# Optimization experiments

Hardware: AMD Instinct MI355X
Metric: run time of the kernel (lower is better)

Reference implementation:

```python
import jax, jax.numpy as jnp
import numpy as np

N = 50_000
E = 1_600_000
C_IN, C_HID, C_OUT, M = 128, 128, 2, 4


def gcn_norm(edge_index, num_nodes):
    # GCNConv default: add self-loops, symmetric normalization D^-1/2 (A+I) D^-1/2
    src, dst = edge_index[0], edge_index[1]
    loop = jnp.arange(num_nodes, dtype=edge_index.dtype)
    src = jnp.concatenate([src, loop])
    dst = jnp.concatenate([dst, loop])
    deg = jax.ops.segment_sum(jnp.ones_like(dst, dtype=jnp.float32), dst,
                              num_segments=num_nodes)
    dinv = jnp.where(deg > 0, jax.lax.rsqrt(deg), 0.0)
    norm = dinv[src] * dinv[dst]  # [E+N]
    return src, dst, norm


def propagate(h, src, dst, norm, num_nodes):
    # gather -> scale -> scatter-add (the memory-bound core)
    return jax.ops.segment_sum(h[src] * norm[:, None], dst, num_segments=num_nodes)


def setup_inputs() -> dict:
    key = jax.random.key(0)
    k0, k1, k2, k3 = jax.random.split(key, 4)
    x = jax.random.normal(k0, (N, C_IN), dtype=jnp.float32)
    edge_index = jax.random.randint(k1, (2, E), 0, N, dtype=jnp.int32)
    W1 = jax.random.normal(k2, (C_IN, C_HID), dtype=jnp.float32) * (1.0 / np.sqrt(C_IN))
    b1 = jnp.zeros((C_HID,), dtype=jnp.float32)
    W_out = jax.random.normal(k3, (M, C_HID, C_OUT), dtype=jnp.float32) * (1.0 / np.sqrt(C_HID))
    b_out = jnp.zeros((M, C_OUT), dtype=jnp.float32)
    return {"x": x, "edge_index": edge_index, "W1": W1, "b1": b1,
            "W_out": W_out, "b_out": b_out}


def reference(x, edge_index, W1, b1, W_out, b_out):
    n = x.shape[0]
    src, dst, norm = gcn_norm(edge_index, n)
    # hidden GCNConv + ReLU
    h = x @ W1                                  # [N, C_HID]
    h = propagate(h, src, dst, norm, n) + b1    # [N, C_HID]
    h = jax.nn.relu(h)
    # m output GCNConv heads. GCN propagation is linear in features, so
    # A_hat(h W_m) == (A_hat h) W_m: share one graph traversal across heads.
    agg = propagate(h, src, dst, norm, n)       # [N, C_HID]
    out = jnp.einsum('nf,mfo->mno', agg, W_out) + b_out[:, None, :]  # [M, N, C_OUT]
    return out
```

## Files before the change

### kernel.cpp

```cpp
#include <hip/hip_runtime.h>


constexpr int CIN = 128;
constexpr int BSHIFT = 6;
constexpr int NBLKB = 256;
constexpr int NBUK_MAX = 1024;
constexpr int CSR_CAP = 4096;

typedef __attribute__((ext_vector_type(8))) short short8v;
typedef __attribute__((ext_vector_type(4))) float float4v;

__device__ inline unsigned pack_bf16x2(float a, float b) {
  unsigned ua = __float_as_uint(a), ub = __float_as_uint(b);
  ua = (ua + 0x7FFFu + ((ua >> 16) & 1u)) >> 16;
  ub = (ub + 0x7FFFu + ((ub >> 16) & 1u)) >> 16;
  return ua | (ub << 16);
}
__device__ inline float bf_lo(unsigned u) { return __uint_as_float(u << 16); }
__device__ inline float bf_hi(unsigned u) { return __uint_as_float(u & 0xFFFF0000u); }

__global__ __launch_bounds__(256) void histbuck_k(const int* __restrict__ dst,
    int* __restrict__ blockhist, int E, int nbuk) {
  __shared__ int lh[NBUK_MAX];
  int b = blockIdx.x, t = threadIdx.x;
  for (int k = t; k < nbuk; k += 256) lh[k] = 0;
  __syncthreads();
  int per = (E + gridDim.x - 1) / gridDim.x;
  int s0 = b * per, s1 = min(E, s0 + per);
  for (int i = s0 + t; i < s1; i += 256) atomicAdd(&lh[dst[i] >> BSHIFT], 1);
  __syncthreads();
  for (int k = t; k < nbuk; k += 256) blockhist[k * NBLKB + b] = lh[k];
}

__global__ void scan_k(const int* __restrict__ v_in,
    int* __restrict__ excl_out, int* __restrict__ btot, int n) {
  __shared__ int wsum[16];
  int t = threadIdx.x, l = t & 63, w = t >> 6;
  int nw = blockDim.x >> 6;
  int i = blockIdx.x * blockDim.x + t;
  int v = (i < n) ? v_in[i] : 0;
  int orig = v;
  #pragma unroll
  for (int off = 1; off < 64; off <<= 1) {
    int u = __shfl_up(v, off);
    if (l >= off) v += u;
  }
  if (l == 63) wsum[w] = v;
  __syncthreads();
  int add = 0;
  for (int j = 0; j < nw; ++j) if (j < w) add += wsum[j];
  v += add;
  if (i < n) excl_out[i] = v - orig;
  if (t == (int)blockDim.x - 1 && btot != nullptr) btot[blockIdx.x] = v;
}

__global__ __launch_bounds__(256) void stageB_k(const int* __restrict__ src,
    const int* __restrict__ dst, const int* __restrict__ soff,
    const int* __restrict__ boff, unsigned* __restrict__ stage, int E, int nbuk) {
  __shared__ int loff[NBUK_MAX];
  int b = blockIdx.x, t = threadIdx.x;
  for (int k = t; k < nbuk; k += 256) loff[k] = soff[k * NBLKB + b] + boff[k];
  __syncthreads();
  int per = (E + gridDim.x - 1) / gridDim.x;
  int s0 = b * per, s1 = min(E, s0 + per);
  for (int i = s0 + t; i < s1; i += 256) {
    int d = dst[i], s = src[i];
    int pos = atomicAdd(&loff[d >> BSHIFT], 1);
    stage[pos] = (unsigned)s | ((unsigned)(d & 63) << 17);
  }
}

__global__ __launch_bounds__(256) void csrloc_k(const unsigned* __restrict__ stage,
    const int* __restrict__ soff, const int* __restrict__ boff,
    int* __restrict__ row_ptr, int* __restrict__ csr,
    float* __restrict__ dinv, int N, int E, int nbuk) {
  __shared__ int cnt64[64], off64[64], cur64[64];
  __shared__ unsigned ebuf[CSR_CAP];
  __shared__ int sbuf[CSR_CAP];
  int k = blockIdx.x, t = threadIdx.x;
  if (t < 64) { cnt64[t] = 0; cur64[t] = 0; }
  __syncthreads();
  int r0 = soff[k * NBLKB] + boff[k];
  int r1 = (k + 1 < nbuk) ? soff[(k + 1) * NBLKB] + boff[k + 1] : E;
  int len = r1 - r0;
  if (len <= CSR_CAP) {
    for (int i = t; i < len; i += 256) {
      unsigned s = stage[r0 + i];
      ebuf[i] = s;
      atomicAdd(&cnt64[s >> 17], 1);
    }
    __syncthreads();
    if (t < 64) {
      int v = cnt64[t], orig = v;
      #pragma unroll
      for (int off = 1; off < 64; off <<= 1) {
        int u = __shfl_up(v, off);
        if (t >= off) v += u;
      }
      off64[t] = v - orig;
      int n = (k << BSHIFT) + t;
      if (n < N) {
        row_ptr[n] = r0 + v - orig;
        dinv[n] = rsqrtf((float)(orig + 1));
      }
      if (k == nbuk - 1 && t == 63) row_ptr[N] = E;
    }
    __syncthreads();
    for (int i = t; i < len; i += 256) {
      unsigned s = ebuf[i];
      int dl = s >> 17;
      int pos = off64[dl] + atomicAdd(&cur64[dl], 1);
      sbuf[pos] = (int)(s & 0x1FFFF);
    }
    __syncthreads();
    for (int i = t; i < len; i += 256) csr[r0 + i] = sbuf[i];
  } else {
    for (int i = r0 + t; i < r1; i += 256) atomicAdd(&cnt64[stage[i] >> 17], 1);
    __syncthreads();
    if (t < 64) {
      int v = cnt64[t], orig = v;
      #pragma unroll
      for (int off = 1; off < 64; off <<= 1) {
        int u = __shfl_up(v, off);
        if (t >= off) v += u;
      }
      off64[t] = v - orig;
      int n = (k << BSHIFT) + t;
      if (n < N) {
        row_ptr[n] = r0 + v - orig;
        dinv[n] = rsqrtf((float)(orig + 1));
      }
      if (k == nbuk - 1 && t == 63) row_ptr[N] = E;
    }
    __syncthreads();
    for (int i = r0 + t; i < r1; i += 256) {
      unsigned s = stage[i];
      int dl = s >> 17;
      int pos = r0 + off64[dl] + atomicAdd(&cur64[dl], 1);
      csr[pos] = (int)(s & 0x1FFFF);
    }
  }
}

__device__ inline void split8(const float* f, short8v& ah, short8v& al) {
  #pragma unroll
  for (int j = 0; j < 8; ++j) {
    unsigned ua = __float_as_uint(f[j]);
    unsigned hb = (ua + 0x7FFFu + ((ua >> 16) & 1u)) >> 16;
    float fh = __uint_as_float(hb << 16);
    float rl = f[j] - fh;
    unsigned ub = __float_as_uint(rl);
    unsigned lb = (ub + 0x7FFFu + ((ub >> 16) & 1u)) >> 16;
    ah[j] = (short)hb;
    al[j] = (short)lb;
  }
}

__global__ __launch_bounds__(256) void gemm_k(const float* __restrict__ x,
    const float* __restrict__ W, const float* __restrict__ dinv,
    unsigned* __restrict__ gu, int nrows) {
  __shared__ unsigned short Bh[16384];
  __shared__ unsigned short Bl[16384];
  int t = threadIdx.x, l = t & 63, w = t >> 6;
  for (int idx = t; idx < 16384; idx += 256) {
    int k = idx >> 7, col = idx & 127;
    float wv = W[idx];
    unsigned ua = __float_as_uint(wv);
    unsigned hb = (ua + 0x7FFFu + ((ua >> 16) & 1u)) >> 16;
    float fh = __uint_as_float(hb << 16);
    float rl = wv - fh;
    unsigned ub = __float_as_uint(rl);
    unsigned lb = (ub + 0x7FFFu + ((ub >> 16) & 1u)) >> 16;
    int addr = (((k >> 5) * 8 + (col >> 4)) * 64 +
                (((k >> 3) & 3) * 16 + (col & 15))) * 8 + (k & 7);
    Bh[addr] = (unsigned short)hb;
    Bl[addr] = (unsigned short)lb;
  }
  __syncthreads();

  int row0 = blockIdx.x * 128;
  int ct0 = w * 2;
  float4v acc[8][2];
  #pragma unroll
  for (int i = 0; i < 8; ++i) { acc[i][0] = (float4v)0.f; acc[i][1] = (float4v)0.f; }
  int arow = row0 + (l & 15);
  int kln = (l >> 4) * 8;

  for (int ks = 0; ks < 4; ++ks) {
    short8v bh0 = *(short8v*)&Bh[((ks * 8 + ct0) * 64 + l) * 8];
    short8v bh1 = *(short8v*)&Bh[((ks * 8 + ct0 + 1) * 64 + l) * 8];
    short8v bl0 = *(short8v*)&Bl[((ks * 8 + ct0) * 64 + l) * 8];
    short8v bl1 = *(short8v*)&Bl[((ks * 8 + ct0 + 1) * 64 + l) * 8];
    #pragma unroll
    for (int rt = 0; rt < 8; ++rt) {
      int r = arow + rt * 16;
      const float* xp = &x[(size_t)min(r, nrows - 1) * CIN + ks * 32 + kln];
      float f[8];
      *(float4*)&f[0] = *(const float4*)xp;
      *(float4*)&f[4] = *(const float4*)(xp + 4);
      short8v ah, al;
      split8(f, ah, al);
      acc[rt][0] = __builtin_amdgcn_mfma_f32_16x16x32_bf16(ah, bh0, acc[rt][0], 0, 0, 0);
      acc[rt][1] = __builtin_amdgcn_mfma_f32_16x16x32_bf16(ah, bh1, acc[rt][1], 0, 0, 0);
      acc[rt][0] = __builtin_amdgcn_mfma_f32_16x16x32_bf16(ah, bl0, acc[rt][0], 0, 0, 0);
      acc[rt][1] = __builtin_amdgcn_mfma_f32_16x16x32_bf16(ah, bl1, acc[rt][1], 0, 0, 0);
      acc[rt][0] = __builtin_amdgcn_mfma_f32_16x16x32_bf16(al, bh0, acc[rt][0], 0, 0, 0);
      acc[rt][1] = __builtin_amdgcn_mfma_f32_16x16x32_bf16(al, bh1, acc[rt][1], 0, 0, 0);
    }
  }
  #pragma unroll
  for (int rt = 0; rt < 8; ++rt) {
    #pragma unroll
    for (int r = 0; r < 4; ++r) {
      int row = row0 + rt * 16 + (l >> 4) * 4 + r;
      bool ok = row < nrows;
      float dv = ok ? dinv[row] : 0.f;
      #pragma unroll
      for (int c = 0; c < 2; ++c) {
        float val = acc[rt][c][r] * dv;
        float other = __shfl_xor(val, 1);
        int col = (ct0 + c) * 16 + (l & 15);
        if (ok && !(l & 1)) gu[(size_t)row * 64 + (col >> 1)] = pack_bf16x2(val, other);
      }
    }
  }
}

#define ACC8(U) do { \
  acc[0] += bf_lo((U).x); acc[1] += bf_hi((U).x); \
  acc[2] += bf_lo((U).y); acc[3] += bf_hi((U).y); \
  acc[4] += bf_lo((U).z); acc[5] += bf_hi((U).z); \
  acc[6] += bf_lo((U).w); acc[7] += bf_hi((U).w); } while (0)

__global__ __launch_bounds__(256) void prop1_k(const uint4* __restrict__ g4,
    const int* __restrict__ row_ptr, const int* __restrict__ csr,
    const float* __restrict__ dinv, const float* __restrict__ b1,
    const float* __restrict__ Wout, unsigned* __restrict__ g2w,
    int n_nodes, int n_waves) {
  int l = threadIdx.x & 63;
  int q = l & 15, sub = l >> 4;
  int wid = (blockIdx.x * blockDim.x + threadIdx.x) >> 6;
  float wj0[8], wj1[8], bb[8];
  #pragma unroll
  for (int c = 0; c < 8; ++c) {
    int col = 8 * q + c;
    wj0[c] = Wout[sub * 256 + col * 2];
    wj1[c] = Wout[sub * 256 + col * 2 + 1];
    bb[c] = b1[col];
  }
  for (int n = wid; n < n_nodes; n += n_waves) {
    int start = row_ptr[n], end = row_ptr[n + 1];
    float d = dinv[n];
    float acc[8];
    #pragma unroll
    for (int c = 0; c < 8; ++c) acc[c] = 0.f;
    for (int base = start; base < end; base += 64) {
      int cnt = min(64, end - base);
      int eb = (base + l < end) ? csr[base + l] : 0;
      int i = 0;
      for (; i + 16 <= cnt; i += 16) {
        int s0 = __shfl(eb, i + sub);
        int s1 = __shfl(eb, i + 4 + sub);
        int s2 = __shfl(eb, i + 8 + sub);
        int s3 = __shfl(eb, i + 12 + sub);
        uint4 u0 = g4[s0 * 16 + q];
        uint4 u1 = g4[s1 * 16 + q];
        uint4 u2 = g4[s2 * 16 + q];
        uint4 u3 = g4[s3 * 16 + q];
        ACC8(u0); ACC8(u1); ACC8(u2); ACC8(u3);
      }
      for (; i + 4 <= cnt; i += 4) {
        int s0 = __shfl(eb, i + sub);
        uint4 u0 = g4[s0 * 16 + q];
        ACC8(u0);
      }
      if (i < cnt) {
        int idx = i + sub;
        bool vld = idx < cnt;
        int s0 = __shfl(eb, vld ? idx : i);
        uint4 u0 = g4[s0 * 16 + q];
        if (vld) { ACC8(u0); }
      }
    }
    #pragma unroll
    for (int c = 0; c < 8; ++c) {
      acc[c] += __shfl_xor(acc[c], 16);
      acc[c] += __shfl_xor(acc[c], 32);
    }
    uint4 us = g4[n * 16 + q];
    ACC8(us);
    float p0 = 0.f, p1 = 0.f;
    #pragma unroll
    for (int c = 0; c < 8; ++c) {
      float y = fmaxf(fmaf(acc[c], d, bb[c]), 0.f);
      p0 = fmaf(y, wj0[c], p0);
      p1 = fmaf(y, wj1[c], p1);
    }
    #pragma unroll
    for (int off = 1; off < 16; off <<= 1) {
      p0 += __shfl_xor(p0, off);
      p1 += __shfl_xor(p1, off);
    }
    if (q == 0) g2w[n * 4 + sub] = pack_bf16x2(d * p0, d * p1);
  }
}

__global__ __launch_bounds__(256) void prop2_k(const uint2* __restrict__ g2v,
    const int* __restrict__ row_ptr, const int* __restrict__ csr,
    const float* __restrict__ dinv, const float* __restrict__ bout,
    float* __restrict__ out, int N) {
  int tid = blockIdx.x * 256 + threadIdx.x;
  int n = tid >> 1, hf = tid & 1;
  if (n >= N) return;
  uint2 us = g2v[n * 2 + hf];
  float a0 = bf_lo(us.x), a1 = bf_hi(us.x);
  float a2 = bf_lo(us.y), a3 = bf_hi(us.y);
  int e = row_ptr[n], e1 = row_ptr[n + 1];
  for (; e + 4 <= e1; e += 4) {
    int i0 = csr[e], i1 = csr[e + 1], i2 = csr[e + 2], i3 = csr[e + 3];
    uint2 u0 = g2v[i0 * 2 + hf], u1 = g2v[i1 * 2 + hf];
    uint2 u2 = g2v[i2 * 2 + hf], u3 = g2v[i3 * 2 + hf];
    a0 += (bf_lo(u0.x) + bf_lo(u1.x)) + (bf_lo(u2.x) + bf_lo(u3.x));
    a1 += (bf_hi(u0.x) + bf_hi(u1.x)) + (bf_hi(u2.x) + bf_hi(u3.x));
    a2 += (bf_lo(u0.y) + bf_lo(u1.y)) + (bf_lo(u2.y) + bf_lo(u3.y));
    a3 += (bf_hi(u0.y) + bf_hi(u1.y)) + (bf_hi(u2.y) + bf_hi(u3.y));
  }
  for (; e < e1; ++e) {
    uint2 u = g2v[csr[e] * 2 + hf];
    a0 += bf_lo(u.x); a1 += bf_hi(u.x);
    a2 += bf_lo(u.y); a3 += bf_hi(u.y);
  }
  float d = dinv[n];
  float2 o0 = make_float2(fmaf(d, a0, bout[hf * 4 + 0]), fmaf(d, a1, bout[hf * 4 + 1]));
  float2 o1 = make_float2(fmaf(d, a2, bout[hf * 4 + 2]), fmaf(d, a3, bout[hf * 4 + 3]));
  *(float2*)&out[(size_t)(hf * 2 + 0) * (2 * N) + 2 * n] = o0;
  *(float2*)&out[(size_t)(hf * 2 + 1) * (2 * N) + 2 * n] = o1;
}

extern "C" void kernel_launch(void* const* d_in, const int* in_sizes, int n_in,
                              void* d_out, int out_size, void* d_ws, size_t ws_size,
                              hipStream_t stream) {
  const float* x    = (const float*)d_in[0];
  const int*   ei   = (const int*)d_in[1];
  const float* W1   = (const float*)d_in[2];
  const float* b1   = (const float*)d_in[3];
  const float* Wout = (const float*)d_in[4];
  const float* bout = (const float*)d_in[5];
  float* out = (float*)d_out;

  const int N = in_sizes[0] / CIN;
  const int E = in_sizes[1] / 2;
  const int* srcp = ei;
  const int* dstp = ei + E;
  const int NBUK = (N + 63) >> BSHIFT;
  const int NSC = NBUK * NBLKB;

  char* ws = (char*)d_ws;
  size_t off = 0;
  auto alloc = [&](size_t bytes) -> void* {
    void* p = ws + off;
    off = (off + bytes + 511) & ~(size_t)511;
    return p;
  };
  unsigned*       gu        = (unsigned*)alloc((size_t)N * 64 * 4);
  unsigned short* g2u       = (unsigned short*)alloc((size_t)N * 8 * 2);
  float*          dinv      = (float*)alloc((size_t)N * 4);
  int*            blockhist = (int*)alloc((size_t)NSC * 4);
  int*            soff      = (int*)alloc((size_t)NSC * 4);
  int*            btot      = (int*)alloc((size_t)NBUK_MAX * 4);
  int*            boff      = (int*)alloc((size_t)NBUK_MAX * 4);
  int*            row_ptr   = (int*)alloc((size_t)(N + 1) * 4);
  int*            csr       = (int*)alloc((size_t)E * 4);
  unsigned*       stage     = (unsigned*)alloc((size_t)E * 4);
  (void)ws_size; (void)n_in; (void)out_size;

  histbuck_k<<<NBLKB, 256, 0, stream>>>(dstp, blockhist, E, NBUK);
  scan_k<<<NBUK, 256, 0, stream>>>(blockhist, soff, btot, NSC);
  scan_k<<<1, 1024, 0, stream>>>(btot, boff, nullptr, NBUK);
  stageB_k<<<NBLKB, 256, 0, stream>>>(srcp, dstp, soff, boff, stage, E, NBUK);
  csrloc_k<<<NBUK, 256, 0, stream>>>(stage, soff, boff, row_ptr, csr, dinv, N, E, NBUK);

  gemm_k<<<(N + 127) / 128, 256, 0, stream>>>(x, W1, dinv, gu, N);

  const int P1_BLOCKS = 2048;
  prop1_k<<<P1_BLOCKS, 256, 0, stream>>>((const uint4*)gu, row_ptr, csr, dinv, b1,
                                         Wout, (unsigned*)g2u, N, P1_BLOCKS * 4);
  prop2_k<<<(2 * N + 255) / 256, 256, 0, stream>>>((const uint2*)g2u, row_ptr, csr,
                                                   dinv, bout, out, N);
}
```

Baseline: 144.1 us.

## Slice hidden features into column panels for cache-local gather and coarsen CSR buckets

The GEMM output is stored as 8 column slices of 16 bf16 features per node, so each gather in the first propagation touches a smaller per-slice table that fits better in L2/LLC. Each block processes one slice, and a new finalize kernel reduces the per-slice partial head projections. CSR construction also moves from 64-node to 256-node buckets with a larger LDS staging buffer. In exchange, the edge list is traversed 8 times, gathers become 32-bit per lane instead of 128-bit, and an fp32 partial buffer plus an extra kernel launch are added.

```diff
diff --git a/kernel.cpp b/kernel.cpp
--- a/kernel.cpp
+++ b/kernel.cpp
@@ -2,10 +2,9 @@
 
 
 constexpr int CIN = 128;
-constexpr int BSHIFT = 6;
+constexpr int SSHIFT = 8;
 constexpr int NBLKB = 256;
-constexpr int NBUK_MAX = 1024;
-constexpr int CSR_CAP = 4096;
+constexpr int CSR_CAP = 10240;
 
 typedef __attribute__((ext_vector_type(8))) short short8v;
 typedef __attribute__((ext_vector_type(4))) float float4v;
@@ -19,17 +18,17 @@
 __device__ inline float bf_lo(unsigned u) { return __uint_as_float(u << 16); }
 __device__ inline float bf_hi(unsigned u) { return __uint_as_float(u & 0xFFFF0000u); }
 
-__global__ __launch_bounds__(256) void histbuck_k(const int* __restrict__ dst,
-    int* __restrict__ blockhist, int E, int nbuk) {
-  __shared__ int lh[NBUK_MAX];
+__global__ __launch_bounds__(256) void histsb_k(const int* __restrict__ dst,
+    int* __restrict__ blockhist, int E, int nsb) {
+  __shared__ int lh[256];
   int b = blockIdx.x, t = threadIdx.x;
-  for (int k = t; k < nbuk; k += 256) lh[k] = 0;
+  lh[t] = 0;
   __syncthreads();
   int per = (E + gridDim.x - 1) / gridDim.x;
   int s0 = b * per, s1 = min(E, s0 + per);
-  for (int i = s0 + t; i < s1; i += 256) atomicAdd(&lh[dst[i] >> BSHIFT], 1);
-  __syncthreads();
-  for (int k = t; k < nbuk; k += 256) blockhist[k * NBLKB + b] = lh[k];
+  for (int i = s0 + t; i < s1; i += 256) atomicAdd(&lh[dst[i] >> SSHIFT], 1);
+  __syncthreads();
+  if (t < nsb) blockhist[t * NBLKB + b] = lh[t];
 }
 
 __global__ void scan_k(const int* __restrict__ v_in,
@@ -56,87 +55,80 @@
 
 __global__ __launch_bounds__(256) void stageB_k(const int* __restrict__ src,
     const int* __restrict__ dst, const int* __restrict__ soff,
-    const int* __restrict__ boff, unsigned* __restrict__ stage, int E, int nbuk) {
-  __shared__ int loff[NBUK_MAX];
+    const int* __restrict__ boff, unsigned* __restrict__ stage, int E, int nsb) {
+  __shared__ int loff[256];
   int b = blockIdx.x, t = threadIdx.x;
-  for (int k = t; k < nbuk; k += 256) loff[k] = soff[k * NBLKB + b] + boff[k];
+  if (t < nsb) loff[t] = soff[t * NBLKB + b] + boff[t];
   __syncthreads();
   int per = (E + gridDim.x - 1) / gridDim.x;
   int s0 = b * per, s1 = min(E, s0 + per);
   for (int i = s0 + t; i < s1; i += 256) {
     int d = dst[i], s = src[i];
-    int pos = atomicAdd(&loff[d >> BSHIFT], 1);
-    stage[pos] = (unsigned)s | ((unsigned)(d & 63) << 17);
-  }
-}
-
-__global__ __launch_bounds__(256) void csrloc_k(const unsigned* __restrict__ stage,
-    const int* __restrict__ soff, const int* __restrict__ boff,
-    int* __restrict__ row_ptr, int* __restrict__ csr,
-    float* __restrict__ dinv, int N, int E, int nbuk) {
-  __shared__ int cnt64[64], off64[64], cur64[64];
+    int pos = atomicAdd(&loff[d >> SSHIFT], 1);
+    stage[pos] = (unsigned)s | ((unsigned)(d & 255) << 17);
+  }
+}
+
+__global__ __launch_bounds__(256) void csrsb_k(const unsigned* __restrict__ stage,
+    const int* __restrict__ boff, int* __restrict__ row_ptr, int* __restrict__ csr,
+    float* __restrict__ dinv, int N, int E, int nsb) {
+  __shared__ int cnt[256], off[256], cur[256];
   __shared__ unsigned ebuf[CSR_CAP];
   __shared__ int sbuf[CSR_CAP];
-  int k = blockIdx.x, t = threadIdx.x;
-  if (t < 64) { cnt64[t] = 0; cur64[t] = 0; }
-  __syncthreads();
-  int r0 = soff[k * NBLKB] + boff[k];
-  int r1 = (k + 1 < nbuk) ? soff[(k + 1) * NBLKB] + boff[k + 1] : E;
+  __shared__ int wsum[4];
+  int k = blockIdx.x, t = threadIdx.x, l = t & 63, w = t >> 6;
+  cnt[t] = 0; cur[t] = 0;
+  __syncthreads();
+  int r0 = boff[k];
+  int r1 = (k + 1 < nsb) ? boff[k + 1] : E;
   int len = r1 - r0;
-  if (len <= CSR_CAP) {
+  bool fits = len <= CSR_CAP;
+  if (fits) {
     for (int i = t; i < len; i += 256) {
       unsigned s = stage[r0 + i];
       ebuf[i] = s;
-      atomicAdd(&cnt64[s >> 17], 1);
-    }
+      atomicAdd(&cnt[s >> 17], 1);
+    }
+  } else {
+    for (int i = r0 + t; i < r1; i += 256) atomicAdd(&cnt[stage[i] >> 17], 1);
+  }
+  __syncthreads();
+  {
+    int v = cnt[t], orig = v;
+    #pragma unroll
+    for (int o = 1; o < 64; o <<= 1) {
+      int u = __shfl_up(v, o);
+      if (l >= o) v += u;
+    }
+    if (l == 63) wsum[w] = v;
     __syncthreads();
-    if (t < 64) {
-      int v = cnt64[t], orig = v;
-      #pragma unroll
-      for (int off = 1; off < 64; off <<= 1) {
-        int u = __shfl_up(v, off);
-        if (t >= off) v += u;
-      }
-      off64[t] = v - orig;
-      int n = (k << BSHIFT) + t;
-      if (n < N) {
-        row_ptr[n] = r0 + v - orig;
-        dinv[n] = rsqrtf((float)(orig + 1));
-      }
-      if (k == nbuk - 1 && t == 63) row_ptr[N] = E;
-    }
-    __syncthreads();
+    int add = 0;
+    #pragma unroll
+    for (int j = 0; j < 4; ++j) if (j < w) add += wsum[j];
+    int excl = v + add - orig;
+    off[t] = excl;
+    int n = (k << SSHIFT) + t;
+    if (n < N) {
+      row_ptr[n] = r0 + excl;
+      dinv[n] = rsqrtf((float)(orig + 1));
+    }
+    if (k == nsb - 1 && t == 255) row_ptr[N] = E;
+  }
+  __syncthreads();
+  if (fits) {
     for (int i = t; i < len; i += 256) {
       unsigned s = ebuf[i];
       int dl = s >> 17;
-      int pos = off64[dl] + atomicAdd(&cur64[dl], 1);
+      int pos = off[dl] + atomicAdd(&cur[dl], 1);
       sbuf[pos] = (int)(s & 0x1FFFF);
     }
     __syncthreads();
     for (int i = t; i < len; i += 256) csr[r0 + i] = sbuf[i];
   } else {
-    for (int i = r0 + t; i < r1; i += 256) atomicAdd(&cnt64[stage[i] >> 17], 1);
-    __syncthreads();
-    if (t < 64) {
-      int v = cnt64[t], orig = v;
-      #pragma unroll
-      for (int off = 1; off < 64; off <<= 1) {
-        int u = __shfl_up(v, off);
-        if (t >= off) v += u;
-      }
-      off64[t] = v - orig;
-      int n = (k << BSHIFT) + t;
-      if (n < N) {
-        row_ptr[n] = r0 + v - orig;
-        dinv[n] = rsqrtf((float)(orig + 1));
-      }
-      if (k == nbuk - 1 && t == 63) row_ptr[N] = E;
-    }
-    __syncthreads();
     for (int i = r0 + t; i < r1; i += 256) {
       unsigned s = stage[i];
       int dl = s >> 17;
-      int pos = r0 + off64[dl] + atomicAdd(&cur64[dl], 1);
+      int pos = r0 + off[dl] + atomicAdd(&cur[dl], 1);
       csr[pos] = (int)(s & 0x1FFFF);
     }
   }
@@ -219,90 +211,86 @@
       for (int c = 0; c < 2; ++c) {
         float val = acc[rt][c][r] * dv;
         float other = __shfl_xor(val, 1);
-        int col = (ct0 + c) * 16 + (l & 15);
-        if (ok && !(l & 1)) gu[(size_t)row * 64 + (col >> 1)] = pack_bf16x2(val, other);
+        int slice = ct0 + c;
+        if (ok && !(l & 1))
+          gu[((size_t)slice * nrows + row) * 8 + ((l & 15) >> 1)] = pack_bf16x2(val, other);
       }
     }
   }
 }
 
-#define ACC8(U) do { \
-  acc[0] += bf_lo((U).x); acc[1] += bf_hi((U).x); \
-  acc[2] += bf_lo((U).y); acc[3] += bf_hi((U).y); \
-  acc[4] += bf_lo((U).z); acc[5] += bf_hi((U).z); \
-  acc[6] += bf_lo((U).w); acc[7] += bf_hi((U).w); } while (0)
-
-__global__ __launch_bounds__(256) void prop1_k(const uint4* __restrict__ g4,
+__global__ __launch_bounds__(256) void prop1s_k(const unsigned* __restrict__ gs,
     const int* __restrict__ row_ptr, const int* __restrict__ csr,
     const float* __restrict__ dinv, const float* __restrict__ b1,
-    const float* __restrict__ Wout, unsigned* __restrict__ g2w,
-    int n_nodes, int n_waves) {
-  int l = threadIdx.x & 63;
-  int q = l & 15, sub = l >> 4;
-  int wid = (blockIdx.x * blockDim.x + threadIdx.x) >> 6;
-  float wj0[8], wj1[8], bb[8];
-  #pragma unroll
-  for (int c = 0; c < 8; ++c) {
-    int col = 8 * q + c;
-    wj0[c] = Wout[sub * 256 + col * 2];
-    wj1[c] = Wout[sub * 256 + col * 2 + 1];
-    bb[c] = b1[col];
-  }
-  for (int n = wid; n < n_nodes; n += n_waves) {
+    const float* __restrict__ Wout, float* __restrict__ g2part,
+    int N, int waves_per_slice) {
+  int slice = blockIdx.x & 7;
+  int chunk = blockIdx.x >> 3;
+  int t = threadIdx.x, l = t & 63, w = t >> 6;
+  int gi = l >> 3, il = l & 7;
+  int c0 = slice * 16 + 2 * il, c1 = c0 + 1;
+  float wa = Wout[(gi >> 1) * 256 + c0 * 2 + (gi & 1)];
+  float wb = Wout[(gi >> 1) * 256 + c1 * 2 + (gi & 1)];
+  float ba = b1[c0], bb2 = b1[c1];
+  const unsigned* gb = gs + (size_t)slice * N * 8 + il;
+  float* gp = g2part + (size_t)slice * N * 8;
+
+  int wsl = chunk * 4 + w;
+  for (int n = wsl; n < N; n += waves_per_slice) {
     int start = row_ptr[n], end = row_ptr[n + 1];
     float d = dinv[n];
-    float acc[8];
-    #pragma unroll
-    for (int c = 0; c < 8; ++c) acc[c] = 0.f;
+    float ax = 0.f, ay = 0.f;
     for (int base = start; base < end; base += 64) {
       int cnt = min(64, end - base);
       int eb = (base + l < end) ? csr[base + l] : 0;
       int i = 0;
       for (; i + 16 <= cnt; i += 16) {
-        int s0 = __shfl(eb, i + sub);
-        int s1 = __shfl(eb, i + 4 + sub);
-        int s2 = __shfl(eb, i + 8 + sub);
-        int s3 = __shfl(eb, i + 12 + sub);
-        uint4 u0 = g4[s0 * 16 + q];
-        uint4 u1 = g4[s1 * 16 + q];
-        uint4 u2 = g4[s2 * 16 + q];
-        uint4 u3 = g4[s3 * 16 + q];
-        ACC8(u0); ACC8(u1); ACC8(u2); ACC8(u3);
+        int sa = __shfl(eb, i + gi);
+        int sb = __shfl(eb, i + 8 + gi);
+        unsigned ua = gb[(size_t)sa * 8];
+        unsigned ub = gb[(size_t)sb * 8];
+        ax += bf_lo(ua) + bf_lo(ub);
+        ay += bf_hi(ua) + bf_hi(ub);
       }
-      for (; i + 4 <= cnt; i += 4) {
-        int s0 = __shfl(eb, i + sub);
-        uint4 u0 = g4[s0 * 16 + q];
-        ACC8(u0);
+      for (; i + 8 <= cnt; i += 8) {
+        int sa = __shfl(eb, i + gi);
+        unsigned ua = gb[(size_t)sa * 8];
+        ax += bf_lo(ua); ay += bf_hi(ua);
       }
       if (i < cnt) {
-        int idx = i + sub;
-        bool vld = idx < cnt;
-        int s0 = __shfl(eb, vld ? idx : i);
-        uint4 u0 = g4[s0 * 16 + q];
-        if (vld) { ACC8(u0); }
+        int idx = i + gi;
+        int sa = __shfl(eb, idx < cnt ? idx : i);
+        if (idx < cnt) {
+          unsigned ua = gb[(size_t)sa * 8];
+          ax += bf_lo(ua); ay += bf_hi(ua);
+        }
       }
     }
-    #pragma unroll
-    for (int c = 0; c < 8; ++c) {
-      acc[c] += __shfl_xor(acc[c], 16);
-      acc[c] += __shfl_xor(acc[c], 32);
-    }
-    uint4 us = g4[n * 16 + q];
-    ACC8(us);
-    float p0 = 0.f, p1 = 0.f;
-    #pragma unroll
-    for (int c = 0; c < 8; ++c) {
-      float y = fmaxf(fmaf(acc[c], d, bb[c]), 0.f);
-      p0 = fmaf(y, wj0[c], p0);
-      p1 = fmaf(y, wj1[c], p1);
-    }
-    #pragma unroll
-    for (int off = 1; off < 16; off <<= 1) {
-      p0 += __shfl_xor(p0, off);
-      p1 += __shfl_xor(p1, off);
-    }
-    if (q == 0) g2w[n * 4 + sub] = pack_bf16x2(d * p0, d * p1);
-  }
+    ax += __shfl_xor(ax, 8); ax += __shfl_xor(ax, 16); ax += __shfl_xor(ax, 32);
+    ay += __shfl_xor(ay, 8); ay += __shfl_xor(ay, 16); ay += __shfl_xor(ay, 32);
+    unsigned us = gb[(size_t)n * 8];
+    ax += bf_lo(us); ay += bf_hi(us);
+    float y0 = fmaxf(fmaf(ax, d, ba), 0.f);
+    float y1 = fmaxf(fmaf(ay, d, bb2), 0.f);
+    float c = fmaf(y0, wa, y1 * wb);
+    c += __shfl_xor(c, 1); c += __shfl_xor(c, 2); c += __shfl_xor(c, 4);
+    if (il == 0) gp[(size_t)n * 8 + gi] = c;
+  }
+}
+
+__global__ __launch_bounds__(256) void finalize_k(const float* __restrict__ g2part,
+    const float* __restrict__ dinv, unsigned* __restrict__ g2w, int N) {
+  int tid = blockIdx.x * 256 + threadIdx.x;
+  if (tid >= N * 4) return;
+  int n = tid >> 2, jp = tid & 3;
+  float s0 = 0.f, s1 = 0.f;
+  #pragma unroll
+  for (int s = 0; s < 8; ++s) {
+    const float* p = &g2part[((size_t)s * N + n) * 8 + jp * 2];
+    s0 += p[0]; s1 += p[1];
+  }
+  float d = dinv[n];
+  g2w[n * 4 + jp] = pack_bf16x2(d * s0, d * s1);
 }
 
 __global__ __launch_bounds__(256) void prop2_k(const uint2* __restrict__ g2v,
@@ -352,8 +340,8 @@
   const int E = in_sizes[1] / 2;
   const int* srcp = ei;
   const int* dstp = ei + E;
-  const int NBUK = (N + 63) >> BSHIFT;
-  const int NSC = NBUK * NBLKB;
+  const int NSB = (N + 255) >> SSHIFT;
+  const int NSC = NSB * NBLKB;
 
   char* ws = (char*)d_ws;
   size_t off = 0;
@@ -363,28 +351,30 @@
     return p;
   };
   unsigned*       gu        = (unsigned*)alloc((size_t)N * 64 * 4);
+  float*          g2part    = (float*)alloc((size_t)8 * N * 8 * 4);
   unsigned short* g2u       = (unsigned short*)alloc((size_t)N * 8 * 2);
   float*          dinv      = (float*)alloc((size_t)N * 4);
   int*            blockhist = (int*)alloc((size_t)NSC * 4);
   int*            soff      = (int*)alloc((size_t)NSC * 4);
-  int*            btot      = (int*)alloc((size_t)NBUK_MAX * 4);
-  int*            boff      = (int*)alloc((size_t)NBUK_MAX * 4);
+  int*            btot      = (int*)alloc(256 * 4);
+  int*            boff      = (int*)alloc(256 * 4);
   int*            row_ptr   = (int*)alloc((size_t)(N + 1) * 4);
   int*            csr       = (int*)alloc((size_t)E * 4);
   unsigned*       stage     = (unsigned*)alloc((size_t)E * 4);
   (void)ws_size; (void)n_in; (void)out_size;
 
-  histbuck_k<<<NBLKB, 256, 0, stream>>>(dstp, blockhist, E, NBUK);
-  scan_k<<<NBUK, 256, 0, stream>>>(blockhist, soff, btot, NSC);
-  scan_k<<<1, 1024, 0, stream>>>(btot, boff, nullptr, NBUK);
-  stageB_k<<<NBLKB, 256, 0, stream>>>(srcp, dstp, soff, boff, stage, E, NBUK);
-  csrloc_k<<<NBUK, 256, 0, stream>>>(stage, soff, boff, row_ptr, csr, dinv, N, E, NBUK);
+  histsb_k<<<NBLKB, 256, 0, stream>>>(dstp, blockhist, E, NSB);
+  scan_k<<<NSB, 256, 0, stream>>>(blockhist, soff, btot, NSC);
+  scan_k<<<1, 256, 0, stream>>>(btot, boff, nullptr, NSB);
+  stageB_k<<<NBLKB, 256, 0, stream>>>(srcp, dstp, soff, boff, stage, E, NSB);
+  csrsb_k<<<NSB, 256, 0, stream>>>(stage, boff, row_ptr, csr, dinv, N, E, NSB);
 
   gemm_k<<<(N + 127) / 128, 256, 0, stream>>>(x, W1, dinv, gu, N);
 
   const int P1_BLOCKS = 2048;
-  prop1_k<<<P1_BLOCKS, 256, 0, stream>>>((const uint4*)gu, row_ptr, csr, dinv, b1,
-                                         Wout, (unsigned*)g2u, N, P1_BLOCKS * 4);
+  prop1s_k<<<P1_BLOCKS, 256, 0, stream>>>(gu, row_ptr, csr, dinv, b1, Wout,
+                                          g2part, N, (P1_BLOCKS / 8) * 4);
+  finalize_k<<<(N * 4 + 255) / 256, 256, 0, stream>>>(g2part, dinv, (unsigned*)g2u, N);
   prop2_k<<<(2 * N + 255) / 256, 256, 0, stream>>>((const uint2*)g2u, row_ptr, csr,
                                                    dinv, bout, out, N);
 }
```

New measurement: 196.1 us. +36.1%, slower.

## Use 256-node superbuckets for CSR build and stage A tiles in LDS

Applied to the files above, without the earlier changes.

The CSR construction now buckets edges by 256-node superbuckets instead of 64-node buckets. This cuts the bucket count to about 196, so the second scan kernel goes away: the bucket-total scan is recomputed inside stageB and the CSR kernel, and the CSR kernel sorts with a 10K-entry LDS buffer. Separately, the GEMM now converts x to bf16 hi/lo once per row into shared memory rather than having each wave reload and split the same x values. The trade-offs are fewer CSR blocks and a larger LDS footprint, which may lower occupancy, plus extra barriers in the GEMM.

```diff
diff --git a/kernel.cpp b/kernel.cpp
--- a/kernel.cpp
+++ b/kernel.cpp
@@ -2,10 +2,9 @@
 
 
 constexpr int CIN = 128;
-constexpr int BSHIFT = 6;
+constexpr int SSHIFT = 8;
 constexpr int NBLKB = 256;
-constexpr int NBUK_MAX = 1024;
-constexpr int CSR_CAP = 4096;
+constexpr int CSR_CAP = 10240;
 
 typedef __attribute__((ext_vector_type(8))) short short8v;
 typedef __attribute__((ext_vector_type(4))) float float4v;
@@ -18,26 +17,34 @@
 }
 __device__ inline float bf_lo(unsigned u) { return __uint_as_float(u << 16); }
 __device__ inline float bf_hi(unsigned u) { return __uint_as_float(u & 0xFFFF0000u); }
-
-__global__ __launch_bounds__(256) void histbuck_k(const int* __restrict__ dst,
-    int* __restrict__ blockhist, int E, int nbuk) {
-  __shared__ int lh[NBUK_MAX];
+__device__ inline void split1(float v, unsigned short& h, unsigned short& lo) {
+  unsigned ua = __float_as_uint(v);
+  unsigned hb = (ua + 0x7FFFu + ((ua >> 16) & 1u)) >> 16;
+  float fh = __uint_as_float(hb << 16);
+  float rl = v - fh;
+  unsigned ub = __float_as_uint(rl);
+  h = (unsigned short)hb;
+  lo = (unsigned short)((ub + 0x7FFFu + ((ub >> 16) & 1u)) >> 16);
+}
+
+__global__ __launch_bounds__(256) void histsb_k(const int* __restrict__ dst,
+    int* __restrict__ blockhist, int E, int nsb) {
+  __shared__ int lh[256];
   int b = blockIdx.x, t = threadIdx.x;
-  for (int k = t; k < nbuk; k += 256) lh[k] = 0;
+  lh[t] = 0;
   __syncthreads();
   int per = (E + gridDim.x - 1) / gridDim.x;
   int s0 = b * per, s1 = min(E, s0 + per);
-  for (int i = s0 + t; i < s1; i += 256) atomicAdd(&lh[dst[i] >> BSHIFT], 1);
-  __syncthreads();
-  for (int k = t; k < nbuk; k += 256) blockhist[k * NBLKB + b] = lh[k];
-}
-
-__global__ void scan_k(const int* __restrict__ v_in,
+  for (int i = s0 + t; i < s1; i += 256) atomicAdd(&lh[dst[i] >> SSHIFT], 1);
+  __syncthreads();
+  if (t < nsb) blockhist[t * NBLKB + b] = lh[t];
+}
+
+__global__ __launch_bounds__(256) void scan_k(const int* __restrict__ v_in,
     int* __restrict__ excl_out, int* __restrict__ btot, int n) {
-  __shared__ int wsum[16];
+  __shared__ int wsum[4];
   int t = threadIdx.x, l = t & 63, w = t >> 6;
-  int nw = blockDim.x >> 6;
-  int i = blockIdx.x * blockDim.x + t;
+  int i = blockIdx.x * 256 + t;
   int v = (i < n) ? v_in[i] : 0;
   int orig = v;
   #pragma unroll
@@ -48,111 +55,114 @@
   if (l == 63) wsum[w] = v;
   __syncthreads();
   int add = 0;
-  for (int j = 0; j < nw; ++j) if (j < w) add += wsum[j];
+  #pragma unroll
+  for (int j = 0; j < 4; ++j) if (j < w) add += wsum[j];
   v += add;
   if (i < n) excl_out[i] = v - orig;
-  if (t == (int)blockDim.x - 1 && btot != nullptr) btot[blockIdx.x] = v;
+  if (t == 255) btot[blockIdx.x] = v;
 }
 
 __global__ __launch_bounds__(256) void stageB_k(const int* __restrict__ src,
     const int* __restrict__ dst, const int* __restrict__ soff,
-    const int* __restrict__ boff, unsigned* __restrict__ stage, int E, int nbuk) {
-  __shared__ int loff[NBUK_MAX];
-  int b = blockIdx.x, t = threadIdx.x;
-  for (int k = t; k < nbuk; k += 256) loff[k] = soff[k * NBLKB + b] + boff[k];
+    const int* __restrict__ btot, unsigned* __restrict__ stage, int E, int nsb) {
+  __shared__ int loff[256];
+  __shared__ int wsum[4];
+  int b = blockIdx.x, t = threadIdx.x, l = t & 63, w = t >> 6;
+  int bv = (t < nsb) ? btot[t] : 0;
+  int vv = bv;
+  #pragma unroll
+  for (int o = 1; o < 64; o <<= 1) { int u = __shfl_up(vv, o); if (l >= o) vv += u; }
+  if (l == 63) wsum[w] = vv;
+  __syncthreads();
+  int add = 0;
+  #pragma unroll
+  for (int j = 0; j < 4; ++j) if (j < w) add += wsum[j];
+  int bexcl = vv + add - bv;
+  if (t < nsb) loff[t] = soff[t * NBLKB + b] + bexcl;
   __syncthreads();
   int per = (E + gridDim.x - 1) / gridDim.x;
   int s0 = b * per, s1 = min(E, s0 + per);
   for (int i = s0 + t; i < s1; i += 256) {
     int d = dst[i], s = src[i];
-    int pos = atomicAdd(&loff[d >> BSHIFT], 1);
-    stage[pos] = (unsigned)s | ((unsigned)(d & 63) << 17);
-  }
-}
-
-__global__ __launch_bounds__(256) void csrloc_k(const unsigned* __restrict__ stage,
-    const int* __restrict__ soff, const int* __restrict__ boff,
-    int* __restrict__ row_ptr, int* __restrict__ csr,
-    float* __restrict__ dinv, int N, int E, int nbuk) {
-  __shared__ int cnt64[64], off64[64], cur64[64];
+    int pos = atomicAdd(&loff[d >> SSHIFT], 1);
+    stage[pos] = (unsigned)s | ((unsigned)(d & 255) << 17);
+  }
+}
+
+__global__ __launch_bounds__(256) void csrsb_k(const unsigned* __restrict__ stage,
+    const int* __restrict__ btot, int* __restrict__ row_ptr, int* __restrict__ csr,
+    float* __restrict__ dinv, int N, int E, int nsb) {
+  __shared__ int cnt[256], off[256], cur[256], sboff[256];
   __shared__ unsigned ebuf[CSR_CAP];
   __shared__ int sbuf[CSR_CAP];
-  int k = blockIdx.x, t = threadIdx.x;
-  if (t < 64) { cnt64[t] = 0; cur64[t] = 0; }
-  __syncthreads();
-  int r0 = soff[k * NBLKB] + boff[k];
-  int r1 = (k + 1 < nbuk) ? soff[(k + 1) * NBLKB] + boff[k + 1] : E;
+  __shared__ int wsum[4];
+  int k = blockIdx.x, t = threadIdx.x, l = t & 63, w = t >> 6;
+  cnt[t] = 0; cur[t] = 0;
+  {
+    int bv = (t < nsb) ? btot[t] : 0;
+    int vv = bv;
+    #pragma unroll
+    for (int o = 1; o < 64; o <<= 1) { int u = __shfl_up(vv, o); if (l >= o) vv += u; }
+    if (l == 63) wsum[w] = vv;
+    __syncthreads();
+    int add = 0;
+    #pragma unroll
+    for (int j = 0; j < 4; ++j) if (j < w) add += wsum[j];
+    sboff[t] = vv + add - bv;
+  }
+  __syncthreads();
+  int r0 = sboff[k];
+  int r1 = (k + 1 < nsb) ? sboff[k + 1] : E;
   int len = r1 - r0;
-  if (len <= CSR_CAP) {
+  bool fits = len <= CSR_CAP;
+  if (fits) {
     for (int i = t; i < len; i += 256) {
       unsigned s = stage[r0 + i];
       ebuf[i] = s;
-      atomicAdd(&cnt64[s >> 17], 1);
-    }
+      atomicAdd(&cnt[s >> 17], 1);
+    }
+  } else {
+    for (int i = r0 + t; i < r1; i += 256) atomicAdd(&cnt[stage[i] >> 17], 1);
+  }
+  __syncthreads();
+  {
+    int v = cnt[t], orig = v;
+    #pragma unroll
+    for (int o = 1; o < 64; o <<= 1) {
+      int u = __shfl_up(v, o);
+      if (l >= o) v += u;
+    }
+    if (l == 63) wsum[w] = v;
     __syncthreads();
-    if (t < 64) {
-      int v = cnt64[t], orig = v;
-      #pragma unroll
-      for (int off = 1; off < 64; off <<= 1) {
-        int u = __shfl_up(v, off);
-        if (t >= off) v += u;
-      }
-      off64[t] = v - orig;
-      int n = (k << BSHIFT) + t;
-      if (n < N) {
-        row_ptr[n] = r0 + v - orig;
-        dinv[n] = rsqrtf((float)(orig + 1));
-      }
-      if (k == nbuk - 1 && t == 63) row_ptr[N] = E;
-    }
-    __syncthreads();
+    int add = 0;
+    #pragma unroll
+    for (int j = 0; j < 4; ++j) if (j < w) add += wsum[j];
+    int excl = v + add - orig;
+    off[t] = excl;
+    int n = (k << SSHIFT) + t;
+    if (n < N) {
+      row_ptr[n] = r0 + excl;
+      dinv[n] = rsqrtf((float)(orig + 1));
+    }
+    if (k == nsb - 1 && t == 255) row_ptr[N] = E;
+  }
+  __syncthreads();
+  if (fits) {
     for (int i = t; i < len; i += 256) {
       unsigned s = ebuf[i];
       int dl = s >> 17;
-      int pos = off64[dl] + atomicAdd(&cur64[dl], 1);
+      int pos = off[dl] + atomicAdd(&cur[dl], 1);
       sbuf[pos] = (int)(s & 0x1FFFF);
     }
     __syncthreads();
     for (int i = t; i < len; i += 256) csr[r0 + i] = sbuf[i];
   } else {
-    for (int i = r0 + t; i < r1; i += 256) atomicAdd(&cnt64[stage[i] >> 17], 1);
-    __syncthreads();
-    if (t < 64) {
-      int v = cnt64[t], orig = v;
-      #pragma unroll
-      for (int off = 1; off < 64; off <<= 1) {
-        int u = __shfl_up(v, off);
-        if (t >= off) v += u;
-      }
-      off64[t] = v - orig;
-      int n = (k << BSHIFT) + t;
-      if (n < N) {
-        row_ptr[n] = r0 + v - orig;
-        dinv[n] = rsqrtf((float)(orig + 1));
-      }
-      if (k == nbuk - 1 && t == 63) row_ptr[N] = E;
-    }
-    __syncthreads();
     for (int i = r0 + t; i < r1; i += 256) {
       unsigned s = stage[i];
       int dl = s >> 17;
-      int pos = r0 + off64[dl] + atomicAdd(&cur64[dl], 1);
+      int pos = r0 + off[dl] + atomicAdd(&cur[dl], 1);
       csr[pos] = (int)(s & 0x1FFFF);
     }
-  }
-}
-
-__device__ inline void split8(const float* f, short8v& ah, short8v& al) {
-  #pragma unroll
-  for (int j = 0; j < 8; ++j) {
-    unsigned ua = __float_as_uint(f[j]);
-    unsigned hb = (ua + 0x7FFFu + ((ua >> 16) & 1u)) >> 16;
-    float fh = __uint_as_float(hb << 16);
-    float rl = f[j] - fh;
-    unsigned ub = __float_as_uint(rl);
-    unsigned lb = (ub + 0x7FFFu + ((ub >> 16) & 1u)) >> 16;
-    ah[j] = (short)hb;
-    al[j] = (short)lb;
   }
 }
 
@@ -161,45 +171,63 @@
     unsigned* __restrict__ gu, int nrows) {
   __shared__ unsigned short Bh[16384];
   __shared__ unsigned short Bl[16384];
+  __shared__ unsigned short Ah[4096];
+  __shared__ unsigned short Al[4096];
   int t = threadIdx.x, l = t & 63, w = t >> 6;
   for (int idx = t; idx < 16384; idx += 256) {
     int k = idx >> 7, col = idx & 127;
-    float wv = W[idx];
-    unsigned ua = __float_as_uint(wv);
-    unsigned hb = (ua + 0x7FFFu + ((ua >> 16) & 1u)) >> 16;
-    float fh = __uint_as_float(hb << 16);
-    float rl = wv - fh;
-    unsigned ub = __float_as_uint(rl);
-    unsigned lb = (ub + 0x7FFFu + ((ub >> 16) & 1u)) >> 16;
+    unsigned short hb, lb;
+    split1(W[idx], hb, lb);
     int addr = (((k >> 5) * 8 + (col >> 4)) * 64 +
                 (((k >> 3) & 3) * 16 + (col & 15))) * 8 + (k & 7);
-    Bh[addr] = (unsigned short)hb;
-    Bl[addr] = (unsigned short)lb;
-  }
-  __syncthreads();
+    Bh[addr] = hb;
+    Bl[addr] = lb;
+  }
 
   int row0 = blockIdx.x * 128;
   int ct0 = w * 2;
   float4v acc[8][2];
   #pragma unroll
   for (int i = 0; i < 8; ++i) { acc[i][0] = (float4v)0.f; acc[i][1] = (float4v)0.f; }
-  int arow = row0 + (l & 15);
-  int kln = (l >> 4) * 8;
+  int arow = l & 15;
+  int kg = l >> 4;
+  int srow = t >> 1, skh = t & 1;
+  int sgrow = min(row0 + srow, nrows - 1);
 
   for (int ks = 0; ks < 4; ++ks) {
+    __syncthreads();
+    {
+      const float* xp = &x[(size_t)sgrow * CIN + ks * 32 + skh * 16];
+      float f[16];
+      *(float4*)&f[0]  = *(const float4*)xp;
+      *(float4*)&f[4]  = *(const float4*)(xp + 4);
+      *(float4*)&f[8]  = *(const float4*)(xp + 8);
+      *(float4*)&f[12] = *(const float4*)(xp + 12);
+      #pragma unroll
+      for (int h = 0; h < 2; ++h) {
+        short8v ah_, al_;
+        #pragma unroll
+        for (int j = 0; j < 8; ++j) {
+          unsigned short hb, lb;
+          split1(f[h * 8 + j], hb, lb);
+          ah_[j] = (short)hb;
+          al_[j] = (short)lb;
+        }
+        int g = skh * 2 + h;
+        *(short8v*)&Ah[(g * 128 + srow) * 8] = ah_;
+        *(short8v*)&Al[(g * 128 + srow) * 8] = al_;
+      }
+    }
+    __syncthreads();
     short8v bh0 = *(short8v*)&Bh[((ks * 8 + ct0) * 64 + l) * 8];
     short8v bh1 = *(short8v*)&Bh[((ks * 8 + ct0 + 1) * 64 + l) * 8];
     short8v bl0 = *(short8v*)&Bl[((ks * 8 + ct0) * 64 + l) * 8];
     short8v bl1 = *(short8v*)&Bl[((ks * 8 + ct0 + 1) * 64 + l) * 8];
     #pragma unroll
     for (int rt = 0; rt < 8; ++rt) {
-      int r = arow + rt * 16;
-      const float* xp = &x[(size_t)min(r, nrows - 1) * CIN + ks * 32 + kln];
-      float f[8];
-      *(float4*)&f[0] = *(const float4*)xp;
-      *(float4*)&f[4] = *(const float4*)(xp + 4);
-      short8v ah, al;
-      split8(f, ah, al);
+      int ar = arow + rt * 16;
+      short8v ah = *(short8v*)&Ah[(kg * 128 + ar) * 8];
+      short8v al = *(short8v*)&Al[(kg * 128 + ar) * 8];
       acc[rt][0] = __builtin_amdgcn_mfma_f32_16x16x32_bf16(ah, bh0, acc[rt][0], 0, 0, 0);
       acc[rt][1] = __builtin_amdgcn_mfma_f32_16x16x32_bf16(ah, bh1, acc[rt][1], 0, 0, 0);
       acc[rt][0] = __builtin_amdgcn_mfma_f32_16x16x32_bf16(ah, bl0, acc[rt][0], 0, 0, 0);
@@ -352,8 +380,8 @@
   const int E = in_sizes[1] / 2;
   const int* srcp = ei;
   const int* dstp = ei + E;
-  const int NBUK = (N + 63) >> BSHIFT;
-  const int NSC = NBUK * NBLKB;
+  const int NSB = (N + 255) >> SSHIFT;
+  const int NSC = NSB * NBLKB;
 
   char* ws = (char*)d_ws;
   size_t off = 0;
@@ -367,18 +395,16 @@
   float*          dinv      = (float*)alloc((size_t)N * 4);
   int*            blockhist = (int*)alloc((size_t)NSC * 4);
   int*            soff      = (int*)alloc((size_t)NSC * 4);
-  int*            btot      = (int*)alloc((size_t)NBUK_MAX * 4);
-  int*            boff      = (int*)alloc((size_t)NBUK_MAX * 4);
+  int*            btot      = (int*)alloc(256 * 4);
   int*            row_ptr   = (int*)alloc((size_t)(N + 1) * 4);
   int*            csr       = (int*)alloc((size_t)E * 4);
   unsigned*       stage     = (unsigned*)alloc((size_t)E * 4);
   (void)ws_size; (void)n_in; (void)out_size;
 
-  histbuck_k<<<NBLKB, 256, 0, stream>>>(dstp, blockhist, E, NBUK);
-  scan_k<<<NBUK, 256, 0, stream>>>(blockhist, soff, btot, NSC);
-  scan_k<<<1, 1024, 0, stream>>>(btot, boff, nullptr, NBUK);
-  stageB_k<<<NBLKB, 256, 0, stream>>>(srcp, dstp, soff, boff, stage, E, NBUK);
-  csrloc_k<<<NBUK, 256, 0, stream>>>(stage, soff, boff, row_ptr, csr, dinv, N, E, NBUK);
+  histsb_k<<<NBLKB, 256, 0, stream>>>(dstp, blockhist, E, NSB);
+  scan_k<<<NSB, 256, 0, stream>>>(blockhist, soff, btot, NSC);
+  stageB_k<<<NBLKB, 256, 0, stream>>>(srcp, dstp, soff, btot, stage, E, NSB);
+  csrsb_k<<<NSB, 256, 0, stream>>>(stage, btot, row_ptr, csr, dinv, N, E, NSB);
 
   gemm_k<<<(N + 127) / 128, 256, 0, stream>>>(x, W1, dinv, gu, N);
 
```

After: 135.8 us. 5.7% less time.
